# Kernel optimization log

Measured on AMD Instinct MI355X. Metric: run time of the kernel, lower is better.

Reference implementation:

```python
import jax, jax.numpy as jnp
import numpy as np

B, N, T, F_FEAT, T_OUT = 256, 512, 12, 12, 12
HID = 3 * N           # 1536, LSTM hidden size
IN = N * F_FEAT       # 6144, LSTM input size


def setup_inputs() -> dict:
    key = jax.random.key(0)
    ks = jax.random.split(key, 8)
    stdv = 1.0 / np.sqrt(HID)
    u = lambda k, shape, s: jax.random.uniform(k, shape, jnp.float32, -s, s)
    return {
        "A_hat": jax.random.normal(ks[0], (N, N), jnp.float32),
        "X": jax.random.normal(ks[1], (B, N, T, F_FEAT), jnp.float32),
        "W_ih": u(ks[2], (4 * HID, IN), stdv),
        "W_hh": u(ks[3], (4 * HID, HID), stdv),
        "b_ih": u(ks[4], (4 * HID,), stdv),
        "b_hh": u(ks[5], (4 * HID,), stdv),
        "lin_W": u(ks[6], (T_OUT, 3 * T), 1.0 / np.sqrt(3 * T)),
        "lin_b": u(ks[7], (T_OUT,), 1.0 / np.sqrt(3 * T)),
    }


def reference(A_hat, X, W_ih, W_hh, b_ih, b_hh, lin_W, lin_b):
    # (B, N, T, F) -> (B, N*T, F) -> (F, B, N*T); loop axis is the feature dim
    out1 = X.reshape(B, N * T, F_FEAT).transpose(2, 0, 1)

    def step(carry, x_t):  # x_t: (B, N*T)
        h, c = carry
        gates = x_t @ W_ih.T + b_ih + h @ W_hh.T + b_hh  # (B, 4*HID)
        i, f, g, o = jnp.split(gates, 4, axis=-1)        # PyTorch gate order i,f,g,o
        c = jax.nn.sigmoid(f) * c + jax.nn.sigmoid(i) * jnp.tanh(g)
        h = jax.nn.sigmoid(o) * jnp.tanh(c)
        h = jnp.tanh(h)  # extra tanh applied in the original forward
        return (h, c), h

    init = (jnp.zeros((B, HID), X.dtype), jnp.zeros((B, HID), X.dtype))
    _, hs = jax.lax.scan(step, init, out1)          # (F, B, HID)
    al = hs.transpose(1, 2, 0)                      # (B, 3N, F) == torch.cat of unsqueezed states
    out2 = al.reshape(B, N, 3 * T)                  # (B, N, 3T)
    out3 = jax.nn.relu(out2) @ lin_W.T + lin_b      # (B, N, T_OUT)
    return out3
```

## Files before the change

### kernel.cpp

```cpp
#include <hip/hip_runtime.h>
#include <hip/hip_bf16.h>
#include <stdint.h>

typedef uint16_t u16;
typedef __attribute__((ext_vector_type(8))) __bf16 bf16x8;
typedef __attribute__((ext_vector_type(4))) float f32x4;
typedef __attribute__((ext_vector_type(4))) u16 u16x4;

#define BSZ   256
#define NN    512
#define TT    12
#define FF    12
#define HID   1536
#define INSZ  6144
#define GATES 6144
#define MROWS 3072
#define SPLITK 2
#define KSPL  (HID / SPLITK)

static __device__ __forceinline__ u16 f2bf(float x) {
  uint32_t u = __builtin_bit_cast(uint32_t, x);
  u += 0x7fffu + ((u >> 16) & 1u);
  return (u16)(u >> 16);
}

static __device__ __forceinline__ float sigm(float x) {
  return 1.0f / (1.0f + expf(-x));
}

__global__ void cvt_bf16(const float* __restrict__ in, u16* __restrict__ out, long n4) {
  long stride = (long)gridDim.x * blockDim.x;
  for (long i = (long)blockIdx.x * blockDim.x + threadIdx.x; i < n4; i += stride) {
    float4 v = ((const float4*)in)[i];
    u16x4 r = { f2bf(v.x), f2bf(v.y), f2bf(v.z), f2bf(v.w) };
    ((u16x4*)out)[i] = r;
  }
}

__global__ void pack_x(const float* __restrict__ X, u16* __restrict__ Ax) {
  int idx = blockIdx.x * blockDim.x + threadIdx.x;
  int b = idx / INSZ;
  int k = idx - b * INSZ;
  const float* xp = X + (size_t)b * (INSZ * FF) + (size_t)k * FF;
  float v[FF];
#pragma unroll
  for (int f = 0; f < FF; ++f) v[f] = xp[f];
#pragma unroll
  for (int f = 0; f < FF; ++f)
    Ax[(size_t)(f * BSZ + b) * INSZ + k] = f2bf(v[f]);
}

#define BM8 192
#define BN8 384
#define LDSA_SZ 24576
#define LDSB_SZ 49152
#define LDS_TOTAL (2 * (LDSA_SZ + LDSB_SZ))

#define GLL(src, dst)                                                          \
  __builtin_amdgcn_global_load_lds(                                            \
      (const __attribute__((address_space(1))) void*)(src),                    \
      (__attribute__((address_space(3))) void*)(dst), 16, 0, 0)

#define SBAR() asm volatile("s_barrier" ::: "memory")
#define SCHED_FENCE_DS() __builtin_amdgcn_sched_barrier(0x7F)

__global__ __launch_bounds__(512, 1) void gemm8p(
    const u16* __restrict__ A, const u16* __restrict__ Bt,
    const float* __restrict__ bi, const float* __restrict__ bh,
    float* __restrict__ C, int M, int N, int K) {
  extern __shared__ __align__(16) char lds[];
  const int tid  = threadIdx.x;
  const int lane = tid & 63;
  const int wid  = tid >> 6;
  const int wr   = wid >> 2;
  const int wc   = wid & 3;

  const int nbx  = N / BN8;
  const int cpx  = gridDim.x >> 3;
  const int orig = blockIdx.x;
  const int wgid = (orig & 7) * cpx + (orig >> 3);
  const int m0   = (wgid / nbx) * BM8;
  const int n0   = (wgid % nbx) * BN8;

  const int fr    = lane & 15;
  const int kb    = (lane >> 4) << 4;
  const int swz   = (fr & 7) << 4;
  const int colp0 = kb ^ swz;
  const int colp1 = (64 | kb) ^ swz;

  const int srow = tid >> 3;
  const int scb  = ((tid & 7) << 4) ^ ((srow & 7) << 4);
  const u16* gA = A  + (size_t)(m0 + srow) * K + (scb >> 1);
  const u16* gB = Bt + (size_t)(n0 + srow) * K + (scb >> 1);
  const int wdst = wid << 10;

  char* ldsA = lds;
  char* ldsB = lds + 2 * LDSA_SZ;
  char* aRowB = ldsA + (wr * 96 + fr) * 128;
  char* bRowB = ldsB + (wc * 96 + fr) * 128;

  f32x4 acc[6][6] = {};
  const int NT = K >> 6;

#pragma unroll
  for (int c = 0; c < 3; ++c) GLL(gA + (size_t)c * 64 * K, ldsA + c * 8192 + wdst);
#pragma unroll
  for (int c = 0; c < 6; ++c) GLL(gB + (size_t)c * 64 * K, ldsB + c * 8192 + wdst);

  for (int t = 0; t < NT; ++t) {
    const int p = t & 1;
    char* aRow = aRowB + p * LDSA_SZ;
    char* bRow = bRowB + p * LDSB_SZ;
    char* An = ldsA + (p ^ 1) * LDSA_SZ;
    char* Bn = ldsB + (p ^ 1) * LDSB_SZ;
    const u16* gAn = gA + (size_t)(t + 1) * 64;
    const u16* gBn = gB + (size_t)(t + 1) * 64;
    const bool pf = (t + 1 < NT);

    bf16x8 a0[2][3], a1[2][3], b0[2][3], b1[2][3];

    if (pf) {
#pragma unroll
      for (int c = 0; c < 3; ++c) GLL(gAn + (size_t)c * 64 * K, An + c * 8192 + wdst);
      asm volatile("s_waitcnt vmcnt(3)" ::: "memory");
    } else {
      asm volatile("s_waitcnt vmcnt(0)" ::: "memory");
    }
    SBAR();

#pragma unroll
    for (int i = 0; i < 3; ++i) {
      a0[0][i] = *(const bf16x8*)(aRow + i * 2048 + colp0);
      a0[1][i] = *(const bf16x8*)(aRow + i * 2048 + colp1);
      b0[0][i] = *(const bf16x8*)(bRow + i * 2048 + colp0);
      b0[1][i] = *(const bf16x8*)(bRow + i * 2048 + colp1);
    }
    __builtin_amdgcn_s_setprio(1);
#pragma unroll
    for (int i = 0; i < 3; ++i)
#pragma unroll
      for (int j = 0; j < 3; ++j) {
        acc[i][j] = __builtin_amdgcn_mfma_f32_16x16x32_bf16(a0[0][i], b0[0][j], acc[i][j], 0, 0, 0);
        acc[i][j] = __builtin_amdgcn_mfma_f32_16x16x32_bf16(a0[1][i], b0[1][j], acc[i][j], 0, 0, 0);
      }
    __builtin_amdgcn_s_setprio(0);
    if (pf) {
      GLL(gBn + (size_t)0 * 64 * K, Bn + 0 * 8192 + wdst);
      GLL(gBn + (size_t)1 * 64 * K, Bn + 1 * 8192 + wdst);
    }
    SCHED_FENCE_DS();

#pragma unroll
    for (int i = 0; i < 3; ++i) {
      b1[0][i] = *(const bf16x8*)(bRow + (3 + i) * 2048 + colp0);
      b1[1][i] = *(const bf16x8*)(bRow + (3 + i) * 2048 + colp1);
    }
    __builtin_amdgcn_s_setprio(1);
#pragma unroll
    for (int i = 0; i < 3; ++i)
#pragma unroll
      for (int j = 0; j < 3; ++j) {
        acc[i][3 + j] = __builtin_amdgcn_mfma_f32_16x16x32_bf16(a0[0][i], b1[0][j], acc[i][3 + j], 0, 0, 0);
        acc[i][3 + j] = __builtin_amdgcn_mfma_f32_16x16x32_bf16(a0[1][i], b1[1][j], acc[i][3 + j], 0, 0, 0);
      }
    __builtin_amdgcn_s_setprio(0);
    if (pf) {
      GLL(gBn + (size_t)2 * 64 * K, Bn + 2 * 8192 + wdst);
      GLL(gBn + (size_t)3 * 64 * K, Bn + 3 * 8192 + wdst);
    }
    SCHED_FENCE_DS();

#pragma unroll
    for (int i = 0; i < 3; ++i) {
      a1[0][i] = *(const bf16x8*)(aRow + (3 + i) * 2048 + colp0);
      a1[1][i] = *(const bf16x8*)(aRow + (3 + i) * 2048 + colp1);
    }
    __builtin_amdgcn_s_setprio(1);
#pragma unroll
    for (int i = 0; i < 3; ++i)
#pragma unroll
      for (int j = 0; j < 3; ++j) {
        acc[3 + i][3 + j] = __builtin_amdgcn_mfma_f32_16x16x32_bf16(a1[0][i], b1[0][j], acc[3 + i][3 + j], 0, 0, 0);
        acc[3 + i][3 + j] = __builtin_amdgcn_mfma_f32_16x16x32_bf16(a1[1][i], b1[1][j], acc[3 + i][3 + j], 0, 0, 0);
      }
    __builtin_amdgcn_s_setprio(0);
    if (pf) {
      GLL(gBn + (size_t)4 * 64 * K, Bn + 4 * 8192 + wdst);
      GLL(gBn + (size_t)5 * 64 * K, Bn + 5 * 8192 + wdst);
    }
    SCHED_FENCE_DS();

    __builtin_amdgcn_s_setprio(1);
#pragma unroll
    for (int i = 0; i < 3; ++i)
#pragma unroll
      for (int j = 0; j < 3; ++j) {
        acc[3 + i][j] = __builtin_amdgcn_mfma_f32_16x16x32_bf16(a1[0][i], b0[0][j], acc[3 + i][j], 0, 0, 0);
        acc[3 + i][j] = __builtin_amdgcn_mfma_f32_16x16x32_bf16(a1[1][i], b0[1][j], acc[3 + i][j], 0, 0, 0);
      }
    __builtin_amdgcn_s_setprio(0);

    SBAR();
  }

  const int r0 = (lane >> 4) << 2;
  const int cc = lane & 15;
#pragma unroll
  for (int j = 0; j < 6; ++j) {
    const int col = n0 + wc * 96 + j * 16 + cc;
    const float bv = bi[col] + bh[col];
#pragma unroll
    for (int i = 0; i < 6; ++i) {
      const size_t rbase = (size_t)(m0 + wr * 96 + i * 16 + r0) * N + col;
#pragma unroll
      for (int r = 0; r < 4; ++r)
        C[rbase + (size_t)r * N] = acc[i][j][r] + bv;
    }
  }
}

#define WAIT_LGKM0()                                                           \
  do {                                                                         \
    asm volatile("s_waitcnt lgkmcnt(0)" ::: "memory");                         \
    __builtin_amdgcn_sched_barrier(0);                                         \
  } while (0)

__global__ __launch_bounds__(256, 4) void gemm_step(
    const u16* __restrict__ A,
    const u16* __restrict__ Bt,
    float* __restrict__ HW) {
  __shared__ __align__(16) char lds[32768];
  const int tid  = threadIdx.x;
  const int lane = tid & 63;
  const int wid  = tid >> 6;
  const int wr   = wid >> 1;
  const int wc   = wid & 1;
  const int n0   = blockIdx.x * 64;
  const int m0   = blockIdx.y * 64;
  const int s    = blockIdx.z;
  const int K    = HID;
  const int koff = s * KSPL;

  const int fr    = lane & 15;
  const int kb    = (lane >> 4) << 4;
  const int swz   = (fr & 7) << 4;
  const int colp0 = kb ^ swz;
  const int colp1 = (64 | kb) ^ swz;

  const int srow = tid >> 3;
  const int scb  = ((tid & 7) << 4) ^ ((srow & 7) << 4);
  const u16* gA = A  + (size_t)(m0 + srow) * K + koff + (scb >> 1);
  const u16* gB = Bt + (size_t)(n0 + srow) * K + koff + (scb >> 1);
  const int wdst = wid << 10;

  char* ldsA = lds;
  char* ldsB = lds + 16384;
  char* aRowB = ldsA + (wr * 32 + fr) * 128;
  char* bRowB = ldsB + (wc * 32 + fr) * 128;

  f32x4 acc[2][2] = {};
  const int NT = KSPL >> 6;

  GLL(gA,                    ldsA + wdst);
  GLL(gA + (size_t)32 * K,   ldsA + 4096 + wdst);
  GLL(gB,                    ldsB + wdst);
  GLL(gB + (size_t)32 * K,   ldsB + 4096 + wdst);

  for (int t = 0; t < NT; ++t) {
    const int p = t & 1;
    char* aRow = aRowB + p * 8192;
    char* bRow = bRowB + p * 8192;
    char* An = ldsA + (p ^ 1) * 8192;
    char* Bn = ldsB + (p ^ 1) * 8192;
    const u16* gAn = gA + (size_t)(t + 1) * 64;
    const u16* gBn = gB + (size_t)(t + 1) * 64;

    if (t + 1 < NT) {
      GLL(gAn,                  An + wdst);
      GLL(gAn + (size_t)32 * K, An + 4096 + wdst);
      GLL(gBn,                  Bn + wdst);
      GLL(gBn + (size_t)32 * K, Bn + 4096 + wdst);
      asm volatile("s_waitcnt vmcnt(4)" ::: "memory");
    } else {
      asm volatile("s_waitcnt vmcnt(0)" ::: "memory");
    }
    SBAR();

    bf16x8 a[2][2], b[2][2];
#pragma unroll
    for (int i = 0; i < 2; ++i) {
      a[0][i] = *(const bf16x8*)(aRow + i * 2048 + colp0);
      a[1][i] = *(const bf16x8*)(aRow + i * 2048 + colp1);
      b[0][i] = *(const bf16x8*)(bRow + i * 2048 + colp0);
      b[1][i] = *(const bf16x8*)(bRow + i * 2048 + colp1);
    }
    WAIT_LGKM0();
    __builtin_amdgcn_s_setprio(1);
#pragma unroll
    for (int i = 0; i < 2; ++i)
#pragma unroll
      for (int j = 0; j < 2; ++j) {
        acc[i][j] = __builtin_amdgcn_mfma_f32_16x16x32_bf16(a[0][i], b[0][j], acc[i][j], 0, 0, 0);
        acc[i][j] = __builtin_amdgcn_mfma_f32_16x16x32_bf16(a[1][i], b[1][j], acc[i][j], 0, 0, 0);
      }
    __builtin_amdgcn_s_setprio(0);
    SBAR();
  }

  float* Cp = HW + (size_t)s * BSZ * GATES;
  const int r0 = (lane >> 4) << 2;
  const int cc = lane & 15;
#pragma unroll
  for (int i = 0; i < 2; ++i)
#pragma unroll
    for (int j = 0; j < 2; ++j) {
      const size_t rbase = (size_t)(m0 + wr * 32 + i * 16 + r0) * GATES +
                           (n0 + wc * 32 + j * 16 + cc);
#pragma unroll
      for (int r = 0; r < 4; ++r)
        Cp[rbase + (size_t)r * GATES] = acc[i][j][r];
    }
}

__global__ void lstm_cell2(const float* __restrict__ XW_f,
                           const float* __restrict__ HWb,
                           float* __restrict__ c,
                           u16* __restrict__ h_bf,
                           float* __restrict__ hs_f,
                           int first) {
  int idx = blockIdx.x * blockDim.x + threadIdx.x;
  int b = idx / (HID / 4);
  int q = idx - b * (HID / 4);
  size_t rowq = (size_t)b * (GATES / 4);

  const float4* xw = (const float4*)XW_f;
  float4 gi = xw[rowq + q];
  float4 gf = xw[rowq + 384 + q];
  float4 gg = xw[rowq + 768 + q];
  float4 go = xw[rowq + 1152 + q];
  float4 cp = {0.f, 0.f, 0.f, 0.f};
  if (!first) {
#pragma unroll
    for (int s = 0; s < SPLITK; ++s) {
      const float4* hg = (const float4*)(HWb + (size_t)s * BSZ * GATES);
      float4 u;
      u = hg[rowq + q];
      gi.x += u.x; gi.y += u.y; gi.z += u.z; gi.w += u.w;
      u = hg[rowq + 384 + q];
      gf.x += u.x; gf.y += u.y; gf.z += u.z; gf.w += u.w;
      u = hg[rowq + 768 + q];
      gg.x += u.x; gg.y += u.y; gg.z += u.z; gg.w += u.w;
      u = hg[rowq + 1152 + q];
      go.x += u.x; go.y += u.y; go.z += u.z; go.w += u.w;
    }
    cp = ((const float4*)c)[idx];
  }
  float4 cn, h;
  {
    float* pi = (float*)&gi; float* pf_ = (float*)&gf; float* pg = (float*)&gg;
    float* po = (float*)&go; float* pc = (float*)&cp;
    float* pcn = (float*)&cn; float* ph = (float*)&h;
#pragma unroll
    for (int e = 0; e < 4; ++e) {
      float cv = sigm(pf_[e]) * pc[e] + sigm(pi[e]) * tanhf(pg[e]);
      pcn[e] = cv;
      ph[e]  = tanhf(sigm(po[e]) * tanhf(cv));
    }
  }
  ((float4*)c)[idx] = cn;
  ((float4*)hs_f)[idx] = h;
  u16x4 hb = { f2bf(h.x), f2bf(h.y), f2bf(h.z), f2bf(h.w) };
  ((u16x4*)h_bf)[idx] = hb;
}

__global__ __launch_bounds__(256) void final_k(const float* __restrict__ hs,
                                               const float* __restrict__ lin_W,
                                               const float* __restrict__ lin_b,
                                               float* __restrict__ out) {
  __shared__ float Wsh[12 * 36];
  __shared__ float bsh[12];
  for (int i = threadIdx.x; i < 12 * 36; i += blockDim.x) Wsh[i] = lin_W[i];
  if (threadIdx.x < 12) bsh[threadIdx.x] = lin_b[threadIdx.x];
  __syncthreads();

  int idx = blockIdx.x * blockDim.x + threadIdx.x;
  int b = idx >> 9;
  int n = idx & 511;

  float acc[12];
#pragma unroll
  for (int o = 0; o < 12; ++o) acc[o] = bsh[o];

#pragma unroll
  for (int kk = 0; kk < 3; ++kk)
#pragma unroll
    for (int f = 0; f < 12; ++f) {
      float v = hs[(size_t)(f * BSZ + b) * HID + 3 * n + kk];
      v = fmaxf(v, 0.0f);
      int j = 12 * kk + f;
#pragma unroll
      for (int o = 0; o < 12; ++o) acc[o] += v * Wsh[o * 36 + j];
    }

#pragma unroll
  for (int o = 0; o < 12; ++o) out[(size_t)idx * 12 + o] = acc[o];
}

extern "C" void kernel_launch(void* const* d_in, const int* in_sizes, int n_in,
                              void* d_out, int out_size, void* d_ws, size_t ws_size,
                              hipStream_t stream) {
  (void)in_sizes; (void)n_in; (void)out_size; (void)ws_size;
  const float* X     = (const float*)d_in[1];
  const float* W_ih  = (const float*)d_in[2];
  const float* W_hh  = (const float*)d_in[3];
  const float* b_ih  = (const float*)d_in[4];
  const float* b_hh  = (const float*)d_in[5];
  const float* lin_W = (const float*)d_in[6];
  const float* lin_b = (const float*)d_in[7];
  float* out = (float*)d_out;

  char* p = (char*)d_ws;
  u16*   Ax   = (u16*)p;   p += (size_t)MROWS * INSZ * 2;
  u16*   Wihb = (u16*)p;   p += (size_t)GATES * INSZ * 2;
  u16*   Whhb = (u16*)p;   p += (size_t)GATES * HID * 2;
  float* XW   = (float*)p; p += (size_t)MROWS * GATES * 4;
  p += (size_t)BSZ * GATES * 4;
  u16*   hbf  = (u16*)p;   p += (size_t)BSZ * HID * 2;
  float* cbuf = (float*)p; p += (size_t)BSZ * HID * 4;
  float* hs   = (float*)p; p += (size_t)FF * BSZ * HID * 4;

  float* HW0 = (float*)Ax;

  hipFuncSetAttribute((const void*)gemm8p,
                      hipFuncAttributeMaxDynamicSharedMemorySize, LDS_TOTAL);

  cvt_bf16<<<4096, 256, 0, stream>>>(W_ih, Wihb, (long)GATES * INSZ / 4);
  cvt_bf16<<<2048, 256, 0, stream>>>(W_hh, Whhb, (long)GATES * HID / 4);
  pack_x<<<(BSZ * INSZ) / 256, 256, 0, stream>>>(X, Ax);

  gemm8p<<<256, 512, LDS_TOTAL, stream>>>(Ax, Wihb, b_ih, b_hh, XW,
                                          MROWS, GATES, INSZ);

  for (int f = 0; f < FF; ++f) {
    if (f > 0)
      gemm_step<<<dim3(GATES / 64, BSZ / 64, SPLITK), 256, 0, stream>>>(hbf, Whhb, HW0);
    lstm_cell2<<<(BSZ * HID / 4) / 256, 256, 0, stream>>>(
        XW + (size_t)f * BSZ * GATES, HW0, cbuf, hbf,
        hs + (size_t)f * BSZ * HID, f == 0 ? 1 : 0);
  }

  final_k<<<(BSZ * NN) / 256, 256, 0, stream>>>(hs, lin_W, lin_b, out);
}
```

Before: 494.4 us.

## Interleave gate rows and fuse recurrent GEMM with LSTM cell epilogue

Permutes W_ih/W_hh rows during bf16 conversion so the i,f,g,o gates of each hidden unit sit in adjacent columns, letting the recurrent GEMM block compute the cell update in its epilogue. Split-K is dropped and the separate lstm_cell kernel with its HW round trip through global memory goes away, and h is double-buffered. It also vectorizes the X packing kernel. The cost is fewer blocks per step (384 instead of 768), each running the full K loop, which may reduce parallelism.

```diff
diff --git a/kernel.cpp b/kernel.cpp
--- a/kernel.cpp
+++ b/kernel.cpp
@@ -15,8 +15,6 @@
 #define INSZ  6144
 #define GATES 6144
 #define MROWS 3072
-#define SPLITK 2
-#define KSPL  (HID / SPLITK)
 
 static __device__ __forceinline__ u16 f2bf(float x) {
   uint32_t u = __builtin_bit_cast(uint32_t, x);
@@ -28,26 +26,32 @@
   return 1.0f / (1.0f + expf(-x));
 }
 
-__global__ void cvt_bf16(const float* __restrict__ in, u16* __restrict__ out, long n4) {
-  long stride = (long)gridDim.x * blockDim.x;
-  for (long i = (long)blockIdx.x * blockDim.x + threadIdx.x; i < n4; i += stride) {
-    float4 v = ((const float4*)in)[i];
-    u16x4 r = { f2bf(v.x), f2bf(v.y), f2bf(v.z), f2bf(v.w) };
-    ((u16x4*)out)[i] = r;
-  }
-}
-
-__global__ void pack_x(const float* __restrict__ X, u16* __restrict__ Ax) {
+__global__ void cvt_perm(const float* __restrict__ in, u16* __restrict__ out,
+                         int ncol4) {
+  long idx = (long)blockIdx.x * blockDim.x + threadIdx.x;
+  int r  = (int)(idx / ncol4);
+  int c4 = (int)(idx - (long)r * ncol4);
+  int rp = ((r % HID) << 2) + r / HID;
+  float4 v = ((const float4*)in)[idx];
+  u16x4 w = { f2bf(v.x), f2bf(v.y), f2bf(v.z), f2bf(v.w) };
+  ((u16x4*)out)[(size_t)rp * ncol4 + c4] = w;
+}
+
+__global__ void pack_x4(const float* __restrict__ X, u16* __restrict__ Ax) {
   int idx = blockIdx.x * blockDim.x + threadIdx.x;
-  int b = idx / INSZ;
-  int k = idx - b * INSZ;
-  const float* xp = X + (size_t)b * (INSZ * FF) + (size_t)k * FF;
-  float v[FF];
-#pragma unroll
-  for (int f = 0; f < FF; ++f) v[f] = xp[f];
-#pragma unroll
-  for (int f = 0; f < FF; ++f)
-    Ax[(size_t)(f * BSZ + b) * INSZ + k] = f2bf(v[f]);
+  int b  = idx / (INSZ / 4);
+  int k4 = idx - b * (INSZ / 4);
+  const float* xp = X + (size_t)b * (INSZ * FF) + (size_t)k4 * (4 * FF);
+  float4 v[12];
+#pragma unroll
+  for (int j = 0; j < 12; ++j) v[j] = ((const float4*)xp)[j];
+  const float* vf = (const float*)v;
+#pragma unroll
+  for (int f = 0; f < FF; ++f) {
+    u16x4 w = { f2bf(vf[0 * FF + f]), f2bf(vf[1 * FF + f]),
+                f2bf(vf[2 * FF + f]), f2bf(vf[3 * FF + f]) };
+    *(u16x4*)&Ax[(size_t)(f * BSZ + b) * INSZ + k4 * 4] = w;
+  }
 }
 
 #define BM8 192
@@ -63,6 +67,11 @@
 
 #define SBAR() asm volatile("s_barrier" ::: "memory")
 #define SCHED_FENCE_DS() __builtin_amdgcn_sched_barrier(0x7F)
+#define WAIT_LGKM0()                                                           \
+  do {                                                                         \
+    asm volatile("s_waitcnt lgkmcnt(0)" ::: "memory");                         \
+    __builtin_amdgcn_sched_barrier(0);                                         \
+  } while (0)
 
 __global__ __launch_bounds__(512, 1) void gemm8p(
     const u16* __restrict__ A, const u16* __restrict__ Bt,
@@ -208,7 +217,8 @@
 #pragma unroll
   for (int j = 0; j < 6; ++j) {
     const int col = n0 + wc * 96 + j * 16 + cc;
-    const float bv = bi[col] + bh[col];
+    const int oc  = (col & 3) * HID + (col >> 2);
+    const float bv = bi[oc] + bh[oc];
 #pragma unroll
     for (int i = 0; i < 6; ++i) {
       const size_t rbase = (size_t)(m0 + wr * 96 + i * 16 + r0) * N + col;
@@ -219,16 +229,13 @@
   }
 }
 
-#define WAIT_LGKM0()                                                           \
-  do {                                                                         \
-    asm volatile("s_waitcnt lgkmcnt(0)" ::: "memory");                         \
-    __builtin_amdgcn_sched_barrier(0);                                         \
-  } while (0)
-
-__global__ __launch_bounds__(256, 4) void gemm_step(
-    const u16* __restrict__ A,
-    const u16* __restrict__ Bt,
-    float* __restrict__ HW) {
+__global__ __launch_bounds__(256, 4) void gemm_cell(
+    const u16* __restrict__ hbf_in,
+    const u16* __restrict__ Whhb,
+    const float* __restrict__ XW_f,
+    float* __restrict__ cbuf,
+    u16* __restrict__ hbf_out,
+    float* __restrict__ hs_f) {
   __shared__ __align__(16) char lds[32768];
   const int tid  = threadIdx.x;
   const int lane = tid & 63;
@@ -237,9 +244,7 @@
   const int wc   = wid & 1;
   const int n0   = blockIdx.x * 64;
   const int m0   = blockIdx.y * 64;
-  const int s    = blockIdx.z;
   const int K    = HID;
-  const int koff = s * KSPL;
 
   const int fr    = lane & 15;
   const int kb    = (lane >> 4) << 4;
@@ -249,8 +254,8 @@
 
   const int srow = tid >> 3;
   const int scb  = ((tid & 7) << 4) ^ ((srow & 7) << 4);
-  const u16* gA = A  + (size_t)(m0 + srow) * K + koff + (scb >> 1);
-  const u16* gB = Bt + (size_t)(n0 + srow) * K + koff + (scb >> 1);
+  const u16* gA = hbf_in + (size_t)(m0 + srow) * K + (scb >> 1);
+  const u16* gB = Whhb   + (size_t)(n0 + srow) * K + (scb >> 1);
   const int wdst = wid << 10;
 
   char* ldsA = lds;
@@ -259,12 +264,12 @@
   char* bRowB = ldsB + (wc * 32 + fr) * 128;
 
   f32x4 acc[2][2] = {};
-  const int NT = KSPL >> 6;
-
-  GLL(gA,                    ldsA + wdst);
-  GLL(gA + (size_t)32 * K,   ldsA + 4096 + wdst);
-  GLL(gB,                    ldsB + wdst);
-  GLL(gB + (size_t)32 * K,   ldsB + 4096 + wdst);
+  const int NT = K >> 6;
+
+  GLL(gA,                  ldsA + wdst);
+  GLL(gA + (size_t)32 * K, ldsA + 4096 + wdst);
+  GLL(gB,                  ldsB + wdst);
+  GLL(gB + (size_t)32 * K, ldsB + 4096 + wdst);
 
   for (int t = 0; t < NT; ++t) {
     const int p = t & 1;
@@ -307,70 +312,55 @@
     SBAR();
   }
 
-  float* Cp = HW + (size_t)s * BSZ * GATES;
+  float* sacc = (float*)lds;
   const int r0 = (lane >> 4) << 2;
   const int cc = lane & 15;
 #pragma unroll
   for (int i = 0; i < 2; ++i)
 #pragma unroll
     for (int j = 0; j < 2; ++j) {
-      const size_t rbase = (size_t)(m0 + wr * 32 + i * 16 + r0) * GATES +
-                           (n0 + wc * 32 + j * 16 + cc);
+      const int ml = wr * 32 + i * 16 + r0;
+      const int nl = wc * 32 + j * 16 + cc;
 #pragma unroll
       for (int r = 0; r < 4; ++r)
-        Cp[rbase + (size_t)r * GATES] = acc[i][j][r];
-    }
-}
-
-__global__ void lstm_cell2(const float* __restrict__ XW_f,
-                           const float* __restrict__ HWb,
-                           float* __restrict__ c,
-                           u16* __restrict__ h_bf,
-                           float* __restrict__ hs_f,
-                           int first) {
-  int idx = blockIdx.x * blockDim.x + threadIdx.x;
-  int b = idx / (HID / 4);
-  int q = idx - b * (HID / 4);
-  size_t rowq = (size_t)b * (GATES / 4);
-
-  const float4* xw = (const float4*)XW_f;
-  float4 gi = xw[rowq + q];
-  float4 gf = xw[rowq + 384 + q];
-  float4 gg = xw[rowq + 768 + q];
-  float4 go = xw[rowq + 1152 + q];
-  float4 cp = {0.f, 0.f, 0.f, 0.f};
-  if (!first) {
-#pragma unroll
-    for (int s = 0; s < SPLITK; ++s) {
-      const float4* hg = (const float4*)(HWb + (size_t)s * BSZ * GATES);
-      float4 u;
-      u = hg[rowq + q];
-      gi.x += u.x; gi.y += u.y; gi.z += u.z; gi.w += u.w;
-      u = hg[rowq + 384 + q];
-      gf.x += u.x; gf.y += u.y; gf.z += u.z; gf.w += u.w;
-      u = hg[rowq + 768 + q];
-      gg.x += u.x; gg.y += u.y; gg.z += u.z; gg.w += u.w;
-      u = hg[rowq + 1152 + q];
-      go.x += u.x; go.y += u.y; go.z += u.z; go.w += u.w;
-    }
-    cp = ((const float4*)c)[idx];
-  }
-  float4 cn, h;
-  {
-    float* pi = (float*)&gi; float* pf_ = (float*)&gf; float* pg = (float*)&gg;
-    float* po = (float*)&go; float* pc = (float*)&cp;
-    float* pcn = (float*)&cn; float* ph = (float*)&h;
-#pragma unroll
-    for (int e = 0; e < 4; ++e) {
-      float cv = sigm(pf_[e]) * pc[e] + sigm(pi[e]) * tanhf(pg[e]);
-      pcn[e] = cv;
-      ph[e]  = tanhf(sigm(po[e]) * tanhf(cv));
-    }
-  }
-  ((float4*)c)[idx] = cn;
-  ((float4*)hs_f)[idx] = h;
-  u16x4 hb = { f2bf(h.x), f2bf(h.y), f2bf(h.z), f2bf(h.w) };
-  ((u16x4*)h_bf)[idx] = hb;
+        sacc[(ml + r) * 68 + nl] = acc[i][j][r];
+    }
+  __syncthreads();
+
+  for (int it = tid; it < 1024; it += 256) {
+    const int bl = it >> 4;
+    const int jl = it & 15;
+    const int b  = m0 + bl;
+    const int jg = (n0 >> 2) + jl;
+    const float4 hw = *(const float4*)&sacc[bl * 68 + jl * 4];
+    const float4 xw = *(const float4*)&XW_f[(size_t)b * GATES + n0 + jl * 4];
+    const float gi = xw.x + hw.x;
+    const float gf = xw.y + hw.y;
+    const float gg = xw.z + hw.z;
+    const float go = xw.w + hw.w;
+    const int cidx = b * HID + jg;
+    const float cp = cbuf[cidx];
+    const float cv = sigm(gf) * cp + sigm(gi) * tanhf(gg);
+    const float h  = tanhf(sigm(go) * tanhf(cv));
+    cbuf[cidx]    = cv;
+    hbf_out[cidx] = f2bf(h);
+    hs_f[cidx]    = h;
+  }
+}
+
+__global__ void cell_first(const float* __restrict__ XW,
+                           float* __restrict__ cbuf,
+                           u16* __restrict__ hbf_out,
+                           float* __restrict__ hs_f) {
+  int it = blockIdx.x * blockDim.x + threadIdx.x;
+  int b = it / HID;
+  int j = it - b * HID;
+  const float4 xw = *(const float4*)&XW[(size_t)b * GATES + 4 * j];
+  const float cv = sigm(xw.x) * tanhf(xw.z);
+  const float h  = tanhf(sigm(xw.w) * tanhf(cv));
+  cbuf[it]    = cv;
+  hbf_out[it] = f2bf(h);
+  hs_f[it]    = h;
 }
 
 __global__ __launch_bounds__(256) void final_k(const float* __restrict__ hs,
@@ -424,29 +414,27 @@
   u16*   Wihb = (u16*)p;   p += (size_t)GATES * INSZ * 2;
   u16*   Whhb = (u16*)p;   p += (size_t)GATES * HID * 2;
   float* XW   = (float*)p; p += (size_t)MROWS * GATES * 4;
-  p += (size_t)BSZ * GATES * 4;
-  u16*   hbf  = (u16*)p;   p += (size_t)BSZ * HID * 2;
+  u16*   hbfA = (u16*)p;   p += (size_t)BSZ * HID * 2;
+  u16*   hbfB = (u16*)p;   p += (size_t)BSZ * HID * 2;
   float* cbuf = (float*)p; p += (size_t)BSZ * HID * 4;
   float* hs   = (float*)p; p += (size_t)FF * BSZ * HID * 4;
 
-  float* HW0 = (float*)Ax;
-
   hipFuncSetAttribute((const void*)gemm8p,
                       hipFuncAttributeMaxDynamicSharedMemorySize, LDS_TOTAL);
 
-  cvt_bf16<<<4096, 256, 0, stream>>>(W_ih, Wihb, (long)GATES * INSZ / 4);
-  cvt_bf16<<<2048, 256, 0, stream>>>(W_hh, Whhb, (long)GATES * HID / 4);
-  pack_x<<<(BSZ * INSZ) / 256, 256, 0, stream>>>(X, Ax);
+  cvt_perm<<<(GATES * (INSZ / 4)) / 256, 256, 0, stream>>>(W_ih, Wihb, INSZ / 4);
+  cvt_perm<<<(GATES * (HID / 4)) / 256, 256, 0, stream>>>(W_hh, Whhb, HID / 4);
+  pack_x4<<<(BSZ * INSZ / 4) / 256, 256, 0, stream>>>(X, Ax);
 
   gemm8p<<<256, 512, LDS_TOTAL, stream>>>(Ax, Wihb, b_ih, b_hh, XW,
                                           MROWS, GATES, INSZ);
 
-  for (int f = 0; f < FF; ++f) {
-    if (f > 0)
-      gemm_step<<<dim3(GATES / 64, BSZ / 64, SPLITK), 256, 0, stream>>>(hbf, Whhb, HW0);
-    lstm_cell2<<<(BSZ * HID / 4) / 256, 256, 0, stream>>>(
-        XW + (size_t)f * BSZ * GATES, HW0, cbuf, hbf,
-        hs + (size_t)f * BSZ * HID, f == 0 ? 1 : 0);
+  u16* bufs[2] = { hbfA, hbfB };
+  cell_first<<<(BSZ * HID) / 256, 256, 0, stream>>>(XW, cbuf, bufs[0], hs);
+  for (int f = 1; f < FF; ++f) {
+    gemm_cell<<<dim3(96, 4), 256, 0, stream>>>(
+        bufs[(f - 1) & 1], Whhb, XW + (size_t)f * BSZ * GATES, cbuf,
+        bufs[f & 1], hs + (size_t)f * BSZ * HID);
   }
 
   final_k<<<(BSZ * NN) / 256, 256, 0, stream>>>(hs, lin_W, lin_b, out);
```

Result: faster. 438.6 us (-11.3%).
